# Performance work log

Hardware: AMD Instinct MI355X
Metric: run time of the kernel (lower is better)

Reference implementation:

```python
import jax, jax.numpy as jnp
import numpy as np

W_BIT = 4
OUT_F = 11008
IN_F = 4096
K = 16
TOKENS = 2048


def unpack_sign(qweight, out_f, in_f):
    """qweight: [w_bit, out_f*in_f//8] ints in [0,256). Each byte packs 8 signs,
    LSB-first: bit j of byte m -> element m*8+j; bit 1 -> +1, bit 0 -> -1.
    Returns float32 signs of shape [w_bit, out_f, in_f]."""
    shifts = jnp.arange(8, dtype=qweight.dtype)
    bits = (qweight[..., None] >> shifts) & 1  # [w_bit, n_bytes, 8]
    sign = (2 * bits - 1).astype(jnp.float32)
    return sign.reshape(qweight.shape[0], out_f, in_f)


def setup_inputs() -> dict:
    key = jax.random.key(0)
    k1, k2, k3, k4 = jax.random.split(key, 4)
    x = jax.random.normal(k1, (TOKENS, IN_F), dtype=jnp.float32)
    qweight = jax.random.randint(k2, (W_BIT, OUT_F * IN_F // 8), 0, 256, dtype=jnp.int32)
    u = jax.random.normal(k3, (W_BIT, OUT_F, K), dtype=jnp.float32) * 0.05
    vt = jax.random.normal(k4, (W_BIT, K, IN_F), dtype=jnp.float32) * 0.05
    return {"x": x, "qweight": qweight, "u": u, "vt": vt}


def reference(x, qweight, u, vt):
    # Reconstruct w = sum_i sign_i * (u_i @ vt_i), then y = x @ w.T  (forward_l0)
    sign = unpack_sign(qweight, OUT_F, IN_F)                  # [b, O, I]
    low_rank = jnp.einsum('bok,bki->boi', u, vt)              # [b, O, I]
    w = jnp.sum(sign * low_rank, axis=0)                      # [O, I]
    return x @ w.T                                            # [T, O]
```

## Files before the change

kernel.cpp:

```cpp
#include <hip/hip_runtime.h>
#include <cstdint>
#include <cstddef>

#define TOKENS 2048
#define IN_F   4096
#define OUT_F  11008
#define W_BIT  4
#define RANK   16
#define QWB    (OUT_F * IN_F / 8)

typedef unsigned short ushort_t;
typedef __attribute__((ext_vector_type(8))) short   short8;
typedef __attribute__((ext_vector_type(4))) float   floatx4;

__device__ __forceinline__ ushort_t f2bf(float f) {
  union { float f; uint32_t u; } c; c.f = f;
  uint32_t r = c.u + 0x7FFFu + ((c.u >> 16) & 1u);
  return (ushort_t)(r >> 16);
}

__device__ __forceinline__ void gl_lds16(const void* g, void* l) {
  __builtin_amdgcn_global_load_lds(
      (const __attribute__((address_space(1))) uint32_t*)g,
      (__attribute__((address_space(3))) uint32_t*)l, 16, 0, 0);
}

__global__ __launch_bounds__(256) void k_cvt_x(const float* __restrict__ x,
                                               ushort_t* __restrict__ xb) {
  int idx = blockIdx.x * 256 + threadIdx.x;
  float4 v = ((const float4*)x)[idx];
  ushort4 r;
  r.x = f2bf(v.x); r.y = f2bf(v.y); r.z = f2bf(v.z); r.w = f2bf(v.w);
  ((ushort4*)xb)[idx] = r;
}

#define N_U  (W_BIT * OUT_F * RANK)
#define N_VT (W_BIT * RANK * IN_F)
__global__ __launch_bounds__(256) void k_prep_uv(const float* __restrict__ u,
                                                 const float* __restrict__ vt,
                                                 ushort_t* __restrict__ ub,
                                                 ushort_t* __restrict__ vtT) {
  int idx = blockIdx.x * 256 + threadIdx.x;
  if (idx < N_U) {
    ub[idx] = f2bf(u[idx]);
  } else {
    int e = idx - N_U;
    int b = e >> 16;
    int r = e & 65535;
    int k = r >> 12;
    int i = r & 4095;
    vtT[((size_t)b * IN_F + i) * RANK + k] = f2bf(vt[e]);
  }
}

__global__ __launch_bounds__(256) void k_build_w(const int* __restrict__ qw,
                                                 const ushort_t* __restrict__ ub,
                                                 const ushort_t* __restrict__ vtT,
                                                 ushort_t* __restrict__ w) {
  __shared__ int qs[W_BIT * 128 * 20];
  const int tid = threadIdx.x;
  const int ob = blockIdx.x / (IN_F / 128);
  const int ib = blockIdx.x % (IN_F / 128);
  const int o0 = ob * 128, i0 = ib * 128;
  const int lane = tid & 63, wv = tid >> 6;
  const int wm = (wv >> 1) * 64, wn = (wv & 1) * 64;
  const int l16 = lane & 15, q = lane >> 4;
  const bool qlo = (q < 2);
  const int koff = (q & 1) * 8;
  const short8 zf = (short8)0;

  #pragma unroll
  for (int n = 0; n < 8; ++n) {
    int c = n * 256 + tid;
    int b = c >> 9, rem = c & 511;
    int row = rem >> 2, part = rem & 3;
    int4 v = *(const int4*)(qw + (size_t)b * QWB +
                            (size_t)(o0 + row) * (IN_F / 8) + (i0 >> 3) + part * 4);
    *(int4*)&qs[(b * 128 + row) * 20 + part * 4] = v;
  }

  floatx4 acc[16];
  #pragma unroll
  for (int i = 0; i < 16; ++i) acc[i] = (floatx4){0.f, 0.f, 0.f, 0.f};

  const int qc_base = (wn >> 3) + (l16 >> 3);
  const int bit = l16 & 7;

  __syncthreads();

  #pragma unroll
  for (int b = 0; b < W_BIT; ++b) {
    short8 af[4], bfr[4];
    #pragma unroll
    for (int mi = 0; mi < 4; ++mi) {
      short8 v = *(const short8*)&ub[((size_t)b * OUT_F + o0 + wm + mi * 16 + l16) * RANK + koff];
      af[mi] = qlo ? v : zf;
    }
    #pragma unroll
    for (int ni = 0; ni < 4; ++ni) {
      short8 v = *(const short8*)&vtT[((size_t)b * IN_F + i0 + wn + ni * 16 + l16) * RANK + koff];
      bfr[ni] = qlo ? v : zf;
    }

    #pragma unroll
    for (int mi = 0; mi < 4; ++mi) {
      floatx4 p[4];
      #pragma unroll
      for (int ni = 0; ni < 4; ++ni)
        p[ni] = __builtin_amdgcn_mfma_f32_16x16x32_bf16(
            af[mi], bfr[ni], (floatx4){0.f, 0.f, 0.f, 0.f}, 0, 0, 0);
      #pragma unroll
      for (int v4 = 0; v4 < 4; ++v4) {
        const int o_loc = wm + mi * 16 + q * 4 + v4;
        const int* qrow = &qs[(b * 128 + o_loc) * 20];
        #pragma unroll
        for (int ni = 0; ni < 4; ++ni) {
          int qv = qrow[qc_base + ni * 2];
          float pv = p[ni][v4];
          acc[mi * 4 + ni][v4] += ((qv >> bit) & 1) ? pv : -pv;
        }
      }
    }
  }

  #pragma unroll
  for (int mi = 0; mi < 4; ++mi) {
    #pragma unroll
    for (int v4 = 0; v4 < 4; ++v4) {
      const int o = o0 + wm + mi * 16 + q * 4 + v4;
      #pragma unroll
      for (int ni = 0; ni < 4; ++ni)
        w[(size_t)o * IN_F + i0 + wn + ni * 16 + l16] = f2bf(acc[mi * 4 + ni][v4]);
    }
  }
}

#define NSTEP (IN_F / 32)
#define SLOT  24576
#define NSLOT 3
__global__ __launch_bounds__(256, 2) void k_gemm_bt(const ushort_t* __restrict__ A,
                                                    const ushort_t* __restrict__ B,
                                                    float* __restrict__ C) {
  __shared__ __attribute__((aligned(16))) char lds[NSLOT * SLOT];
  const int tid = threadIdx.x;
  const int wg = (blockIdx.x & 7) * 86 + (blockIdx.x >> 3);
  const int bm = wg & 7;
  const int bn = wg >> 3;
  const int lane = tid & 63, wv = tid >> 6;
  const int wm = wv >> 1, wn = wv & 1;
  const int l16 = lane & 15, q = lane >> 4;
  const int sQ = q ^ ((l16 >> 1) & 3);

  const size_t ar = (size_t)bm * 256, br = (size_t)bn * 128;
  const int qsrc = (tid & 3) ^ ((tid >> 3) & 3);
  const ushort_t* Ae = A + (ar + (tid >> 2)) * IN_F + qsrc * 8;
  const ushort_t* Be = B + (br + (tid >> 2)) * IN_F + qsrc * 8;
  const int ldsoff = (tid & 192) * 16;
  const int aFrag = (wm * 128 + l16) * 64 + sQ * 16;
  const int bFrag = (wn * 64 + l16) * 64 + sQ * 16;

  floatx4 acc[8][4];
  #pragma unroll
  for (int mi = 0; mi < 8; ++mi)
    #pragma unroll
    for (int ni = 0; ni < 4; ++ni) acc[mi][ni] = (floatx4){0.f, 0.f, 0.f, 0.f};

  short8 af[8], bf[4];
  int sLd = 0;
  int sWr = 2 * SLOT;

#define STAGEK(kt, off) do {                                                 \
    const size_t _k0 = (size_t)(kt) * 32;                                    \
    char* _d = lds + (off) + ldsoff;                                         \
    gl_lds16(Ae + _k0,                 _d);                                  \
    gl_lds16(Ae +  64 * IN_F + _k0,    _d + 4096);                           \
    gl_lds16(Ae + 128 * IN_F + _k0,    _d + 8192);                           \
    gl_lds16(Ae + 192 * IN_F + _k0,    _d + 12288);                          \
    gl_lds16(Be + _k0,                 _d + 16384);                          \
    gl_lds16(Be +  64 * IN_F + _k0,    _d + 20480);                          \
  } while (0)

#define PHASE(u_, VM, DO_STAGE) do {                                         \
    asm volatile(VM ::: "memory");                                           \
    __builtin_amdgcn_s_barrier();                                            \
    asm volatile("" ::: "memory");                                           \
    {                                                                        \
      const char* _ab = lds + sLd;                                           \
      const char* _bb = _ab + 16384;                                         \
      _Pragma("unroll") for (int mi = 0; mi < 8; ++mi)                       \
        af[mi] = *(const short8*)(_ab + aFrag + mi * 1024);                  \
      _Pragma("unroll") for (int ni = 0; ni < 4; ++ni)                       \
        bf[ni] = *(const short8*)(_bb + bFrag + ni * 1024);                  \
    }                                                                        \
    if (DO_STAGE) STAGEK((u_) + 2, sWr);                                     \
    __builtin_amdgcn_s_setprio(1);                                           \
    _Pragma("unroll") for (int mi = 0; mi < 8; ++mi)                         \
      _Pragma("unroll") for (int ni = 0; ni < 4; ++ni)                       \
        acc[mi][ni] = __builtin_amdgcn_mfma_f32_16x16x32_bf16(               \
            af[mi], bf[ni], acc[mi][ni], 0, 0, 0);                           \
    __builtin_amdgcn_s_setprio(0);                                           \
    sLd += SLOT; if (sLd == NSLOT * SLOT) sLd = 0;                           \
    sWr += SLOT; if (sWr == NSLOT * SLOT) sWr = 0;                           \
  } while (0)

  STAGEK(0, 0); STAGEK(1, SLOT);

  for (int u = 0; u < NSTEP - 2; ++u)
    PHASE(u, "s_waitcnt vmcnt(6)", true);
  PHASE(NSTEP - 2, "s_waitcnt vmcnt(6)", false);
  PHASE(NSTEP - 1, "s_waitcnt vmcnt(0)", false);

#undef STAGEK
#undef PHASE

  #pragma unroll
  for (int mi = 0; mi < 8; ++mi) {
    #pragma unroll
    for (int ni = 0; ni < 4; ++ni) {
      #pragma unroll
      for (int v = 0; v < 4; ++v) {
        int r = bm * 256 + wm * 128 + mi * 16 + q * 4 + v;
        int c = bn * 128 + wn * 64 + ni * 16 + l16;
        C[(size_t)r * OUT_F + c] = acc[mi][ni][v];
      }
    }
  }
}

extern "C" void kernel_launch(void* const* d_in, const int* in_sizes, int n_in,
                              void* d_out, int out_size, void* d_ws, size_t ws_size,
                              hipStream_t stream) {
  (void)in_sizes; (void)n_in; (void)out_size; (void)ws_size;
  const float* x  = (const float*)d_in[0];
  const int*   qw = (const int*)d_in[1];
  const float* u  = (const float*)d_in[2];
  const float* vt = (const float*)d_in[3];
  float* out = (float*)d_out;

  char* wsp = (char*)d_ws;
  ushort_t* xb  = (ushort_t*)wsp;
  ushort_t* wb  = (ushort_t*)(wsp + (size_t)TOKENS * IN_F * 2);
  ushort_t* ubf = (ushort_t*)(wsp + (size_t)TOKENS * IN_F * 2 + (size_t)OUT_F * IN_F * 2);
  ushort_t* vtT = (ushort_t*)(wsp + (size_t)TOKENS * IN_F * 2 + (size_t)OUT_F * IN_F * 2 +
                              (size_t)N_U * 2);

  k_cvt_x<<<TOKENS * IN_F / 1024, 256, 0, stream>>>(x, xb);
  k_prep_uv<<<(N_U + N_VT) / 256, 256, 0, stream>>>(u, vt, ubf, vtT);
  k_build_w<<<(OUT_F / 128) * (IN_F / 128), 256, 0, stream>>>(qw, ubf, vtT, wb);
  k_gemm_bt<<<8 * (OUT_F / 128), 256, 0, stream>>>(xb, wb, out);
}
```

Measured before the change: 422.1 us.

## Enlarge GEMM tile to 256x256 with 8 waves and split-phase LDS pipeline

The bf16 GEMM block tile grows from 256x128 to 256x256. Each block now runs 512 threads (8 waves in a 2x4 layout), and each LDS slot grows to 32KB. Every k-step is split into two half-phases: the first half-phase stages A and runs the MFMAs for the upper A fragments, the second stages B and runs the lower A fragments, with barriers around each half. The aim is to raise operand reuse per global load and interleave prefetch with compute more finely. The cost is extra barriers, 96KB of LDS per block (likely one block per CU), and fewer, larger blocks that may leave a worse tail across CUs.

```diff
diff --git a/kernel.cpp b/kernel.cpp
--- a/kernel.cpp
+++ b/kernel.cpp
@@ -136,26 +136,26 @@
 }
 
 #define NSTEP (IN_F / 32)
-#define SLOT  24576
+#define SLOT  32768
 #define NSLOT 3
-__global__ __launch_bounds__(256, 2) void k_gemm_bt(const ushort_t* __restrict__ A,
+__global__ __launch_bounds__(512, 2) void k_gemm_bt(const ushort_t* __restrict__ A,
                                                     const ushort_t* __restrict__ B,
                                                     float* __restrict__ C) {
   __shared__ __attribute__((aligned(16))) char lds[NSLOT * SLOT];
   const int tid = threadIdx.x;
-  const int wg = (blockIdx.x & 7) * 86 + (blockIdx.x >> 3);
+  const int wg = (blockIdx.x & 7) * 43 + (blockIdx.x >> 3);
   const int bm = wg & 7;
   const int bn = wg >> 3;
   const int lane = tid & 63, wv = tid >> 6;
-  const int wm = wv >> 1, wn = wv & 1;
+  const int wm = wv >> 2, wn = wv & 3;
   const int l16 = lane & 15, q = lane >> 4;
   const int sQ = q ^ ((l16 >> 1) & 3);
 
-  const size_t ar = (size_t)bm * 256, br = (size_t)bn * 128;
+  const size_t ar = (size_t)bm * 256, br = (size_t)bn * 256;
   const int qsrc = (tid & 3) ^ ((tid >> 3) & 3);
   const ushort_t* Ae = A + (ar + (tid >> 2)) * IN_F + qsrc * 8;
   const ushort_t* Be = B + (br + (tid >> 2)) * IN_F + qsrc * 8;
-  const int ldsoff = (tid & 192) * 16;
+  const int ldsoff = (tid & 448) * 16;
   const int aFrag = (wm * 128 + l16) * 64 + sQ * 16;
   const int bFrag = (wn * 64 + l16) * 64 + sQ * 16;
 
@@ -165,53 +165,89 @@
     #pragma unroll
     for (int ni = 0; ni < 4; ++ni) acc[mi][ni] = (floatx4){0.f, 0.f, 0.f, 0.f};
 
-  short8 af[8], bf[4];
-  int sLd = 0;
-  int sWr = 2 * SLOT;
-
-#define STAGEK(kt, off) do {                                                 \
+  short8 af0[4], af1[4], bf[4];
+  int sRd = 0, sWr = 2 * SLOT;
+
+#define STAGE_A(kt, off) do {                                                \
     const size_t _k0 = (size_t)(kt) * 32;                                    \
     char* _d = lds + (off) + ldsoff;                                         \
-    gl_lds16(Ae + _k0,                 _d);                                  \
-    gl_lds16(Ae +  64 * IN_F + _k0,    _d + 4096);                           \
-    gl_lds16(Ae + 128 * IN_F + _k0,    _d + 8192);                           \
-    gl_lds16(Ae + 192 * IN_F + _k0,    _d + 12288);                          \
-    gl_lds16(Be + _k0,                 _d + 16384);                          \
-    gl_lds16(Be +  64 * IN_F + _k0,    _d + 20480);                          \
-  } while (0)
-
-#define PHASE(u_, VM, DO_STAGE) do {                                         \
-    asm volatile(VM ::: "memory");                                           \
-    __builtin_amdgcn_s_barrier();                                            \
-    asm volatile("" ::: "memory");                                           \
+    gl_lds16(Ae + _k0,                _d);                                   \
+    gl_lds16(Ae + 128 * IN_F + _k0,   _d + 8192);                            \
+  } while (0)
+
+#define STAGE_B(kt, off) do {                                                \
+    const size_t _k0 = (size_t)(kt) * 32;                                    \
+    char* _d = lds + (off) + 16384 + ldsoff;                                 \
+    gl_lds16(Be + _k0,                _d);                                   \
+    gl_lds16(Be + 128 * IN_F + _k0,   _d + 8192);                            \
+  } while (0)
+
+#define PHASE0(t_, DO_STAGE) do {                                            \
     {                                                                        \
-      const char* _ab = lds + sLd;                                           \
+      const char* _ab = lds + sRd;                                           \
       const char* _bb = _ab + 16384;                                         \
-      _Pragma("unroll") for (int mi = 0; mi < 8; ++mi)                       \
-        af[mi] = *(const short8*)(_ab + aFrag + mi * 1024);                  \
+      _Pragma("unroll") for (int mi = 0; mi < 4; ++mi)                       \
+        af0[mi] = *(const short8*)(_ab + aFrag + mi * 1024);                 \
       _Pragma("unroll") for (int ni = 0; ni < 4; ++ni)                       \
         bf[ni] = *(const short8*)(_bb + bFrag + ni * 1024);                  \
     }                                                                        \
-    if (DO_STAGE) STAGEK((u_) + 2, sWr);                                     \
+    if (DO_STAGE) STAGE_A((t_) + 2, sWr);                                    \
+    asm volatile("" ::: "memory");                                           \
+    __builtin_amdgcn_s_barrier();                                            \
+    asm volatile("" ::: "memory");                                           \
     __builtin_amdgcn_s_setprio(1);                                           \
-    _Pragma("unroll") for (int mi = 0; mi < 8; ++mi)                         \
+    _Pragma("unroll") for (int mi = 0; mi < 4; ++mi)                         \
       _Pragma("unroll") for (int ni = 0; ni < 4; ++ni)                       \
         acc[mi][ni] = __builtin_amdgcn_mfma_f32_16x16x32_bf16(               \
-            af[mi], bf[ni], acc[mi][ni], 0, 0, 0);                           \
+            af0[mi], bf[ni], acc[mi][ni], 0, 0, 0);                          \
     __builtin_amdgcn_s_setprio(0);                                           \
-    sLd += SLOT; if (sLd == NSLOT * SLOT) sLd = 0;                           \
+    asm volatile("" ::: "memory");                                           \
+    __builtin_amdgcn_s_barrier();                                            \
+    asm volatile("" ::: "memory");                                           \
+  } while (0)
+
+#define PHASE1(t_, DO_STAGE, VM) do {                                        \
+    {                                                                        \
+      const char* _ab = lds + sRd;                                           \
+      _Pragma("unroll") for (int mi = 0; mi < 4; ++mi)                       \
+        af1[mi] = *(const short8*)(_ab + aFrag + (4 + mi) * 1024);           \
+    }                                                                        \
+    if (DO_STAGE) STAGE_B((t_) + 2, sWr);                                    \
+    asm volatile(VM ::: "memory");       \
+    __builtin_amdgcn_s_barrier();                                            \
+    asm volatile("" ::: "memory");                                           \
+    __builtin_amdgcn_s_setprio(1);                                           \
+    _Pragma("unroll") for (int mi = 0; mi < 4; ++mi)                         \
+      _Pragma("unroll") for (int ni = 0; ni < 4; ++ni)                       \
+        acc[4 + mi][ni] = __builtin_amdgcn_mfma_f32_16x16x32_bf16(           \
+            af1[mi], bf[ni], acc[4 + mi][ni], 0, 0, 0);                      \
+    __builtin_amdgcn_s_setprio(0);                                           \
+    asm volatile("" ::: "memory");                                           \
+    __builtin_amdgcn_s_barrier();                                            \
+    asm volatile("" ::: "memory");                                           \
+    sRd += SLOT; if (sRd == NSLOT * SLOT) sRd = 0;                           \
     sWr += SLOT; if (sWr == NSLOT * SLOT) sWr = 0;                           \
   } while (0)
 
-  STAGEK(0, 0); STAGEK(1, SLOT);
-
-  for (int u = 0; u < NSTEP - 2; ++u)
-    PHASE(u, "s_waitcnt vmcnt(6)", true);
-  PHASE(NSTEP - 2, "s_waitcnt vmcnt(6)", false);
-  PHASE(NSTEP - 1, "s_waitcnt vmcnt(0)", false);
-
-#undef STAGEK
-#undef PHASE
+  STAGE_A(0, 0); STAGE_B(0, 0);
+  STAGE_A(1, SLOT); STAGE_B(1, SLOT);
+  asm volatile("s_waitcnt vmcnt(4)" ::: "memory");
+  __builtin_amdgcn_s_barrier();
+  asm volatile("" ::: "memory");
+
+  for (int t = 0; t < NSTEP - 2; ++t) {
+    PHASE0(t, true);
+    PHASE1(t, true, "s_waitcnt vmcnt(4)");
+  }
+  PHASE0(NSTEP - 2, false);
+  PHASE1(NSTEP - 2, false, "s_waitcnt vmcnt(0)");
+  PHASE0(NSTEP - 1, false);
+  PHASE1(NSTEP - 1, false, "s_waitcnt vmcnt(0)");
+
+#undef STAGE_A
+#undef STAGE_B
+#undef PHASE0
+#undef PHASE1
 
   #pragma unroll
   for (int mi = 0; mi < 8; ++mi) {
@@ -220,7 +256,7 @@
       #pragma unroll
       for (int v = 0; v < 4; ++v) {
         int r = bm * 256 + wm * 128 + mi * 16 + q * 4 + v;
-        int c = bn * 128 + wn * 64 + ni * 16 + l16;
+        int c = bn * 256 + wn * 64 + ni * 16 + l16;
         C[(size_t)r * OUT_F + c] = acc[mi][ni][v];
       }
     }
@@ -247,5 +283,5 @@
   k_cvt_x<<<TOKENS * IN_F / 1024, 256, 0, stream>>>(x, xb);
   k_prep_uv<<<(N_U + N_VT) / 256, 256, 0, stream>>>(u, vt, ubf, vtT);
   k_build_w<<<(OUT_F / 128) * (IN_F / 128), 256, 0, stream>>>(qw, ubf, vtT, wb);
-  k_gemm_bt<<<8 * (OUT_F / 128), 256, 0, stream>>>(xb, wb, out);
-}
+  k_gemm_bt<<<8 * (OUT_F / 256), 512, 0, stream>>>(xb, wb, out);
+}
```

Result: slower. 451.8 us (+7.0%).
